# Kernel optimization log

Measured on AMD Instinct MI355X. Metric: run time of the kernel, lower is better.

Reference implementation:

```python
import jax, jax.numpy as jnp
import numpy as np

N_NODES = 50000
N_EDGES = 800000
M_IN = 512
H_OUT = 512


def setup_inputs() -> dict:
    key = jax.random.key(0)
    k1, k2, k3, k4, k5 = jax.random.split(key, 5)
    X = jax.random.normal(k1, (N_NODES, M_IN), dtype=jnp.float32)
    # Xavier-uniform init like nn.init.xavier_uniform_
    limit = float(np.sqrt(6.0 / (M_IN + H_OUT)))
    W = jax.random.uniform(k2, (M_IN, H_OUT), dtype=jnp.float32, minval=-limit, maxval=limit)
    edge_src = jax.random.randint(k3, (N_EDGES,), 0, N_NODES, dtype=jnp.int64 if jax.config.jax_enable_x64 else jnp.int32)
    edge_dst = jax.random.randint(k4, (N_EDGES,), 0, N_NODES, dtype=jnp.int64 if jax.config.jax_enable_x64 else jnp.int32)
    # positive normalized-adjacency-like weights
    edge_vals = jax.random.uniform(k5, (N_EDGES,), dtype=jnp.float32, minval=0.0, maxval=1.0)
    return {"X": X, "W": W, "edge_src": edge_src, "edge_dst": edge_dst, "edge_vals": edge_vals}


def reference(X, W, edge_src, edge_dst, edge_vals):
    # Z = X @ W   (dense projection)
    Z = jnp.matmul(X, W)  # [N, h]
    # A_hat @ Z via COO SpMM: gather source rows, scale by edge weight, scatter-add to dst
    msg = Z[edge_src] * edge_vals[:, None]          # [E, h]
    agg = jax.ops.segment_sum(msg, edge_dst, num_segments=X.shape[0])  # [N, h]
    # sigma = ReLU
    return jax.nn.relu(agg)
```

## Files before the change

### kernel.cpp

```cpp
#include <hip/hip_runtime.h>
#include <hip/hip_bf16.h>

#define N_NODES 50000
#define N_EDGES 800000
#define M_IN 512
#define H_OUT 512
#define BCAP 64

typedef __attribute__((ext_vector_type(8))) short    bf16x8;
typedef __attribute__((ext_vector_type(4))) float    f32x4;
typedef __attribute__((ext_vector_type(8))) unsigned short u16x8;

__device__ inline float bf2f(unsigned short u) {
    unsigned int x = ((unsigned int)u) << 16;
    return __builtin_bit_cast(float, x);
}
__device__ inline unsigned short f2bf(float f) {
    unsigned int x = __builtin_bit_cast(unsigned int, f);
    return (unsigned short)((x + 0x7FFF + ((x >> 16) & 1)) >> 16);
}
__device__ inline void gload_lds16(const void* g, void* lds) {
    __builtin_amdgcn_global_load_lds(
        (const __attribute__((address_space(1))) void*)g,
        (__attribute__((address_space(3))) void*)lds, 16, 0, 0);
}

#define PREP_GROUPS 1042
#define PREP_GRID   (PREP_GROUPS * 10)
#define CONVX_B 6250
#define CONVW_B 1024
#define BUILD_B 3125

__global__ __launch_bounds__(256) void prep_kernel(
    const float* __restrict__ X, unsigned char* __restrict__ Xq,
    float* __restrict__ sc,
    const float* __restrict__ W, unsigned short* __restrict__ Wt,
    const int* __restrict__ esrc, const int* __restrict__ edst,
    const float* __restrict__ eval,
    int* __restrict__ cnt, unsigned int* __restrict__ pairs)
{
    const int grp = blockIdx.x / 10;
    const int ph  = blockIdx.x % 10;
    if (ph < 6) {
        const int cb = grp * 6 + ph;
        if (cb >= CONVX_B) return;
        const int r0 = (cb * 4 + (threadIdx.x >> 6)) * 2;
        const int l  = threadIdx.x & 63;

        const float4 a0 = *(const float4*)(X + (size_t)r0 * M_IN + l * 8);
        const float4 b0 = *(const float4*)(X + (size_t)r0 * M_IN + l * 8 + 4);
        const float4 a1 = *(const float4*)(X + (size_t)(r0 + 1) * M_IN + l * 8);
        const float4 b1 = *(const float4*)(X + (size_t)(r0 + 1) * M_IN + l * 8 + 4);

        float m0 = fmaxf(fmaxf(fmaxf(fabsf(a0.x), fabsf(a0.y)), fmaxf(fabsf(a0.z), fabsf(a0.w))),
                         fmaxf(fmaxf(fabsf(b0.x), fabsf(b0.y)), fmaxf(fabsf(b0.z), fabsf(b0.w))));
        float m1 = fmaxf(fmaxf(fmaxf(fabsf(a1.x), fabsf(a1.y)), fmaxf(fabsf(a1.z), fabsf(a1.w))),
                         fmaxf(fmaxf(fabsf(b1.x), fabsf(b1.y)), fmaxf(fabsf(b1.z), fabsf(b1.w))));
#pragma unroll
        for (int d = 1; d < 64; d <<= 1) {
            m0 = fmaxf(m0, __shfl_xor(m0, d, 64));
            m1 = fmaxf(m1, __shfl_xor(m1, d, 64));
        }
        const float inv0 = (m0 > 0.f) ? 127.f / m0 : 0.f;
        const float inv1 = (m1 > 0.f) ? 127.f / m1 : 0.f;

        const float xs0[8] = {a0.x, a0.y, a0.z, a0.w, b0.x, b0.y, b0.z, b0.w};
        const float xs1[8] = {a1.x, a1.y, a1.z, a1.w, b1.x, b1.y, b1.z, b1.w};
        unsigned int u0[8], u1[8];
#pragma unroll
        for (int j = 0; j < 8; ++j) {
            int q0 = __float2int_rn(xs0[j] * inv0) + 128;
            int q1 = __float2int_rn(xs1[j] * inv1) + 128;
            u0[j] = (unsigned int)max(0, min(255, q0));
            u1[j] = (unsigned int)max(0, min(255, q1));
        }
        uint2 w0, w1;
        w0.x = u0[0] | (u0[1] << 8) | (u0[2] << 16) | (u0[3] << 24);
        w0.y = u0[4] | (u0[5] << 8) | (u0[6] << 16) | (u0[7] << 24);
        w1.x = u1[0] | (u1[1] << 8) | (u1[2] << 16) | (u1[3] << 24);
        w1.y = u1[4] | (u1[5] << 8) | (u1[6] << 16) | (u1[7] << 24);
        *(uint2*)(Xq + (size_t)r0 * M_IN + l * 8)       = w0;
        *(uint2*)(Xq + (size_t)(r0 + 1) * M_IN + l * 8) = w1;
        if (l == 0) sc[r0] = m0 * (1.f / 127.f);
        if (l == 1) sc[r0 + 1] = m1 * (1.f / 127.f);
    } else if (ph < 9) {
        const int bb = grp * 3 + (ph - 6);
        if (bb >= BUILD_B) return;
        const int e = bb * 256 + threadIdx.x;
        const int d   = edst[e];
        const int pos = atomicAdd(&cnt[d], 1);
        if (pos < BCAP)
            pairs[(size_t)d * BCAP + pos] =
                ((unsigned int)esrc[e] << 16) | (unsigned int)f2bf(eval[e]);
    } else {
        const int wb = grp;
        if (wb >= CONVW_B) return;
        const int id = wb * 256 + threadIdx.x;
        const int n = id >> 9, k = id & 511;
        Wt[(size_t)n * 512 + k] = f2bf(W[(size_t)k * 512 + n]);
    }
}

__global__ __launch_bounds__(256) void gather_kernel(
    const unsigned char* __restrict__ Xq,
    const float*        __restrict__ sc,
    const int*          __restrict__ cnt,
    const unsigned int* __restrict__ pairs,
    unsigned short*     __restrict__ Yb)
{
    const int node = blockIdx.x * 4 + (threadIdx.x >> 6);
    const int lane = threadIdx.x & 63;

    const int beg = node * BCAP;
    const int end = beg + min(cnt[node], BCAP);
    const int col = lane * 8;

    float acc[8] = {};
    float S = 0.f;

    int e = beg;
    for (; e + 3 < end; e += 4) {
        const unsigned int k0 = pairs[e],     k1 = pairs[e + 1];
        const unsigned int k2 = pairs[e + 2], k3 = pairs[e + 3];
        const uint2 x0 = *(const uint2*)(Xq + (size_t)(k0 >> 16) * M_IN + col);
        const uint2 x1 = *(const uint2*)(Xq + (size_t)(k1 >> 16) * M_IN + col);
        const uint2 x2 = *(const uint2*)(Xq + (size_t)(k2 >> 16) * M_IN + col);
        const uint2 x3 = *(const uint2*)(Xq + (size_t)(k3 >> 16) * M_IN + col);
        const float f0 = bf2f((unsigned short)(k0 & 0xffffu)) * sc[k0 >> 16];
        const float f1 = bf2f((unsigned short)(k1 & 0xffffu)) * sc[k1 >> 16];
        const float f2 = bf2f((unsigned short)(k2 & 0xffffu)) * sc[k2 >> 16];
        const float f3 = bf2f((unsigned short)(k3 & 0xffffu)) * sc[k3 >> 16];
        S += f0 + f1 + f2 + f3;
#pragma unroll
        for (int j = 0; j < 4; ++j) {
            acc[j]     += (float)((x0.x >> (8 * j)) & 0xffu) * f0
                        + (float)((x1.x >> (8 * j)) & 0xffu) * f1
                        + (float)((x2.x >> (8 * j)) & 0xffu) * f2
                        + (float)((x3.x >> (8 * j)) & 0xffu) * f3;
            acc[4 + j] += (float)((x0.y >> (8 * j)) & 0xffu) * f0
                        + (float)((x1.y >> (8 * j)) & 0xffu) * f1
                        + (float)((x2.y >> (8 * j)) & 0xffu) * f2
                        + (float)((x3.y >> (8 * j)) & 0xffu) * f3;
        }
    }
    for (; e < end; ++e) {
        const unsigned int k0 = pairs[e];
        const uint2 x0 = *(const uint2*)(Xq + (size_t)(k0 >> 16) * M_IN + col);
        const float f0 = bf2f((unsigned short)(k0 & 0xffffu)) * sc[k0 >> 16];
        S += f0;
#pragma unroll
        for (int j = 0; j < 4; ++j) {
            acc[j]     += (float)((x0.x >> (8 * j)) & 0xffu) * f0;
            acc[4 + j] += (float)((x0.y >> (8 * j)) & 0xffu) * f0;
        }
    }

    u16x8 o;
#pragma unroll
    for (int j = 0; j < 8; ++j) o[j] = f2bf(acc[j] - 128.f * S);
    *(u16x8*)(Yb + (size_t)node * M_IN + col) = o;
}

#define BM 128
#define BN 128
#define BK 32
#define NT (M_IN / BK)
#define ROWT ((N_NODES + BM - 1) / BM)
#define GEMM_GRID (((ROWT + 7) / 8) * 8 * 4)

__global__ __launch_bounds__(256, 4) void gemm_mfma_kernel(
    const unsigned short* __restrict__ Yb,
    const unsigned short* __restrict__ Wt,
    float* __restrict__ out)
{
    const int bid = blockIdx.x;
    const int s   = bid >> 3;
    const int r   = (s >> 2) * 8 + (bid & 7);
    if (r >= ROWT) return;
    const int row0 = r * BM;
    const int col0 = (s & 3) * BN;

    __shared__ unsigned short As[2][BM * BK];
    __shared__ unsigned short Bs[2][BN * BK];

    const int tid  = threadIdx.x;
    const int lane = tid & 63;
    const int wid  = tid >> 6;
    const int wr   = wid >> 1;
    const int wc   = wid & 1;

    f32x4 acc[4][4] = {};

    int srow[2], ksw[2], ldsb[2];
#pragma unroll
    for (int i = 0; i < 2; ++i) {
        const int b   = (i * 256 + tid) * 16;
        const int row = b >> 6;
        const int cir = (b >> 4) & 3;
        srow[i] = row;
        ksw[i]  = (cir ^ ((row >> 1) & 3)) << 3;
        ldsb[i] = b;
    }
    int agr[2];
#pragma unroll
    for (int i = 0; i < 2; ++i) {
        int gr = row0 + srow[i];
        if (gr >= N_NODES) gr = N_NODES - 1;
        agr[i] = gr;
    }

    int abyte[4], bbyte[4];
    const int c = lane >> 4;
#pragma unroll
    for (int m = 0; m < 4; ++m) {
        const int ra = wr * 64 + m * 16 + (lane & 15);
        abyte[m] = ra * 64 + ((c ^ ((ra >> 1) & 3)) << 4);
        const int rb = wc * 64 + m * 16 + (lane & 15);
        bbyte[m] = rb * 64 + ((c ^ ((rb >> 1) & 3)) << 4);
    }

#define STAGE(buf, k0)                                                          \
    do {                                                                        \
        _Pragma("unroll")                                                       \
        for (int i = 0; i < 2; ++i) {                                           \
            gload_lds16(Yb + (size_t)agr[i] * M_IN + (k0) + ksw[i],             \
                        (char*)As[buf] + ldsb[i]);                              \
            gload_lds16(Wt + (size_t)(col0 + srow[i]) * M_IN + (k0) + ksw[i],   \
                        (char*)Bs[buf] + ldsb[i]);                              \
        }                                                                       \
    } while (0)

    STAGE(0, 0);
    asm volatile("s_waitcnt vmcnt(0)" ::: "memory");
    __builtin_amdgcn_s_barrier();

    int cur = 0;
    for (int t = 0; t < NT; ++t) {
        if (t + 1 < NT) STAGE(cur ^ 1, (t + 1) * BK);

        bf16x8 af[4], bfr[4];
#pragma unroll
        for (int m = 0; m < 4; ++m)
            af[m]  = *(const bf16x8*)((const char*)As[cur] + abyte[m]);
#pragma unroll
        for (int n = 0; n < 4; ++n)
            bfr[n] = *(const bf16x8*)((const char*)Bs[cur] + bbyte[n]);

#pragma unroll
        for (int m = 0; m < 4; ++m)
#pragma unroll
            for (int n = 0; n < 4; ++n)
                acc[m][n] = __builtin_amdgcn_mfma_f32_16x16x32_bf16(
                    af[m], bfr[n], acc[m][n], 0, 0, 0);

        if (t + 1 < NT) {
            asm volatile("s_waitcnt vmcnt(0)" ::: "memory");
            __builtin_amdgcn_s_barrier();
        }
        cur ^= 1;
    }
#undef STAGE

#pragma unroll
    for (int m = 0; m < 4; ++m) {
#pragma unroll
        for (int n = 0; n < 4; ++n) {
#pragma unroll
            for (int rr = 0; rr < 4; ++rr) {
                const int row = row0 + wr * 64 + m * 16 + (lane >> 4) * 4 + rr;
                const int col = col0 + wc * 64 + n * 16 + (lane & 15);
                if (row < N_NODES)
                    out[(size_t)row * H_OUT + col] = fmaxf(acc[m][n][rr], 0.f);
            }
        }
    }
}

extern "C" void kernel_launch(void* const* d_in, const int* in_sizes, int n_in,
                              void* d_out, int out_size, void* d_ws, size_t ws_size,
                              hipStream_t stream) {
    const float* X    = (const float*)d_in[0];
    const float* W    = (const float*)d_in[1];
    const int*   esrc = (const int*)d_in[2];
    const int*   edst = (const int*)d_in[3];
    const float* eval = (const float*)d_in[4];
    float* out = (float*)d_out;

    char* w = (char*)d_ws;
    unsigned short* Yb = (unsigned short*)w;  w += (size_t)N_NODES * M_IN * 2;
    unsigned char*  Xq = (unsigned char*)w;   w += (size_t)N_NODES * M_IN;
    float*          sc = (float*)w;           w += (size_t)N_NODES * 4;
    unsigned short* Wt = (unsigned short*)w;  w += (size_t)M_IN * H_OUT * 2;
    int*   cnt  = (int*)w;                    w += (size_t)N_NODES * 4;
    unsigned int* pairs = (unsigned int*)w;

    hipMemsetAsync(cnt, 0, (size_t)N_NODES * sizeof(int), stream);

    prep_kernel<<<PREP_GRID, 256, 0, stream>>>(
        X, Xq, sc, W, Wt, esrc, edst, eval, cnt, pairs);

    gather_kernel<<<(N_NODES + 3) / 4, 256, 0, stream>>>(Xq, sc, cnt, pairs, Yb);

    gemm_mfma_kernel<<<GEMM_GRID, 256, 0, stream>>>(Yb, Wt, out);
}
```

Before: 164.6 us.

## Switch aggregation GEMM from bf16 to int8 MFMA with per-row/column scales

Quantizes the aggregated features to int8 with a per-node scale in the gather kernel, and quantizes W to int8 with a per-output-column scale. The GEMM then uses i32 16x16x64 int8 MFMA with BK=64 and dequantizes in the epilogue. This halves operand bytes for Yq and W and uses the higher-throughput int8 matrix path. The cost is a wavefront max-reduction in the gather, extra scale loads in the epilogue, and lower numerical accuracy from 8-bit quantization of both operands.

```diff
diff --git a/kernel.cpp b/kernel.cpp
--- a/kernel.cpp
+++ b/kernel.cpp
@@ -7,8 +7,7 @@
 #define H_OUT 512
 #define BCAP 64
 
-typedef __attribute__((ext_vector_type(8))) short    bf16x8;
-typedef __attribute__((ext_vector_type(4))) float    f32x4;
+typedef __attribute__((ext_vector_type(4))) int      v4i;
 typedef __attribute__((ext_vector_type(8))) unsigned short u16x8;
 
 __device__ inline float bf2f(unsigned short u) {
@@ -28,13 +27,14 @@
 #define PREP_GROUPS 1042
 #define PREP_GRID   (PREP_GROUPS * 10)
 #define CONVX_B 6250
-#define CONVW_B 1024
 #define BUILD_B 3125
+#define WQ_B    128
 
 __global__ __launch_bounds__(256) void prep_kernel(
     const float* __restrict__ X, unsigned char* __restrict__ Xq,
     float* __restrict__ sc,
-    const float* __restrict__ W, unsigned short* __restrict__ Wt,
+    const float* __restrict__ W, signed char* __restrict__ Wq,
+    float* __restrict__ sw,
     const int* __restrict__ esrc, const int* __restrict__ edst,
     const float* __restrict__ eval,
     int* __restrict__ cnt, unsigned int* __restrict__ pairs)
@@ -93,11 +93,28 @@
             pairs[(size_t)d * BCAP + pos] =
                 ((unsigned int)esrc[e] << 16) | (unsigned int)f2bf(eval[e]);
     } else {
-        const int wb = grp;
-        if (wb >= CONVW_B) return;
-        const int id = wb * 256 + threadIdx.x;
-        const int n = id >> 9, k = id & 511;
-        Wt[(size_t)n * 512 + k] = f2bf(W[(size_t)k * 512 + n]);
+        if (grp >= WQ_B) return;
+        const int n = grp * 4 + (threadIdx.x >> 6);
+        const int l = threadIdx.x & 63;
+        float wv[8];
+        float am = 0.f;
+#pragma unroll
+        for (int j = 0; j < 8; ++j) {
+            wv[j] = W[(size_t)(l * 8 + j) * H_OUT + n];
+            am = fmaxf(am, fabsf(wv[j]));
+        }
+#pragma unroll
+        for (int d = 1; d < 64; d <<= 1) am = fmaxf(am, __shfl_xor(am, d, 64));
+        const float inv = (am > 0.f) ? 127.f / am : 0.f;
+        int q[8];
+#pragma unroll
+        for (int j = 0; j < 8; ++j)
+            q[j] = max(-127, min(127, __float2int_rn(wv[j] * inv)));
+        uint2 pk;
+        pk.x = (q[0] & 0xff) | ((q[1] & 0xff) << 8) | ((q[2] & 0xff) << 16) | ((q[3] & 0xff) << 24);
+        pk.y = (q[4] & 0xff) | ((q[5] & 0xff) << 8) | ((q[6] & 0xff) << 16) | ((q[7] & 0xff) << 24);
+        *(uint2*)(Wq + (size_t)n * M_IN + l * 8) = pk;
+        if (l == 0) sw[n] = am * (1.f / 127.f);
     }
 }
 
@@ -106,7 +123,8 @@
     const float*        __restrict__ sc,
     const int*          __restrict__ cnt,
     const unsigned int* __restrict__ pairs,
-    unsigned short*     __restrict__ Yb)
+    signed char*        __restrict__ Yq,
+    float*              __restrict__ sy)
 {
     const int node = blockIdx.x * 4 + (threadIdx.x >> 6);
     const int lane = threadIdx.x & 63;
@@ -155,22 +173,39 @@
         }
     }
 
-    u16x8 o;
-#pragma unroll
-    for (int j = 0; j < 8; ++j) o[j] = f2bf(acc[j] - 128.f * S);
-    *(u16x8*)(Yb + (size_t)node * M_IN + col) = o;
+    float y[8];
+    float am = 0.f;
+#pragma unroll
+    for (int j = 0; j < 8; ++j) {
+        y[j] = acc[j] - 128.f * S;
+        am = fmaxf(am, fabsf(y[j]));
+    }
+#pragma unroll
+    for (int d = 1; d < 64; d <<= 1) am = fmaxf(am, __shfl_xor(am, d, 64));
+    const float inv = (am > 0.f) ? 127.f / am : 0.f;
+    int q[8];
+#pragma unroll
+    for (int j = 0; j < 8; ++j)
+        q[j] = max(-127, min(127, __float2int_rn(y[j] * inv)));
+    uint2 pk;
+    pk.x = (q[0] & 0xff) | ((q[1] & 0xff) << 8) | ((q[2] & 0xff) << 16) | ((q[3] & 0xff) << 24);
+    pk.y = (q[4] & 0xff) | ((q[5] & 0xff) << 8) | ((q[6] & 0xff) << 16) | ((q[7] & 0xff) << 24);
+    *(uint2*)(Yq + (size_t)node * M_IN + col) = pk;
+    if (lane == 0) sy[node] = am * (1.f / 127.f);
 }
 
 #define BM 128
 #define BN 128
-#define BK 32
-#define NT (M_IN / BK)
+#define BKI 64
+#define NTI (M_IN / BKI)
 #define ROWT ((N_NODES + BM - 1) / BM)
 #define GEMM_GRID (((ROWT + 7) / 8) * 8 * 4)
 
-__global__ __launch_bounds__(256, 4) void gemm_mfma_kernel(
-    const unsigned short* __restrict__ Yb,
-    const unsigned short* __restrict__ Wt,
+__global__ __launch_bounds__(256, 4) void gemm_i8_kernel(
+    const signed char* __restrict__ Yq,
+    const signed char* __restrict__ Wq,
+    const float* __restrict__ sy,
+    const float* __restrict__ sw,
     float* __restrict__ out)
 {
     const int bid = blockIdx.x;
@@ -180,8 +215,8 @@
     const int row0 = r * BM;
     const int col0 = (s & 3) * BN;
 
-    __shared__ unsigned short As[2][BM * BK];
-    __shared__ unsigned short Bs[2][BN * BK];
+    __shared__ signed char As[2][BM * BKI];
+    __shared__ signed char Bs[2][BN * BKI];
 
     const int tid  = threadIdx.x;
     const int lane = tid & 63;
@@ -189,7 +224,7 @@
     const int wr   = wid >> 1;
     const int wc   = wid & 1;
 
-    f32x4 acc[4][4] = {};
+    v4i acc[4][4] = {};
 
     int srow[2], ksw[2], ldsb[2];
 #pragma unroll
@@ -198,7 +233,7 @@
         const int row = b >> 6;
         const int cir = (b >> 4) & 3;
         srow[i] = row;
-        ksw[i]  = (cir ^ ((row >> 1) & 3)) << 3;
+        ksw[i]  = (cir ^ ((row >> 1) & 3)) << 4;
         ldsb[i] = b;
     }
     int agr[2];
@@ -223,9 +258,9 @@
     do {                                                                        \
         _Pragma("unroll")                                                       \
         for (int i = 0; i < 2; ++i) {                                           \
-            gload_lds16(Yb + (size_t)agr[i] * M_IN + (k0) + ksw[i],             \
+            gload_lds16(Yq + (size_t)agr[i] * M_IN + (k0) + ksw[i],             \
                         (char*)As[buf] + ldsb[i]);                              \
-            gload_lds16(Wt + (size_t)(col0 + srow[i]) * M_IN + (k0) + ksw[i],   \
+            gload_lds16(Wq + (size_t)(col0 + srow[i]) * M_IN + (k0) + ksw[i],   \
                         (char*)Bs[buf] + ldsb[i]);                              \
         }                                                                       \
     } while (0)
@@ -235,25 +270,25 @@
     __builtin_amdgcn_s_barrier();
 
     int cur = 0;
-    for (int t = 0; t < NT; ++t) {
-        if (t + 1 < NT) STAGE(cur ^ 1, (t + 1) * BK);
-
-        bf16x8 af[4], bfr[4];
+    for (int t = 0; t < NTI; ++t) {
+        if (t + 1 < NTI) STAGE(cur ^ 1, (t + 1) * BKI);
+
+        v4i af[4], bfr[4];
 #pragma unroll
         for (int m = 0; m < 4; ++m)
-            af[m]  = *(const bf16x8*)((const char*)As[cur] + abyte[m]);
+            af[m]  = *(const v4i*)((const char*)As[cur] + abyte[m]);
 #pragma unroll
         for (int n = 0; n < 4; ++n)
-            bfr[n] = *(const bf16x8*)((const char*)Bs[cur] + bbyte[n]);
+            bfr[n] = *(const v4i*)((const char*)Bs[cur] + bbyte[n]);
 
 #pragma unroll
         for (int m = 0; m < 4; ++m)
 #pragma unroll
             for (int n = 0; n < 4; ++n)
-                acc[m][n] = __builtin_amdgcn_mfma_f32_16x16x32_bf16(
+                acc[m][n] = __builtin_amdgcn_mfma_i32_16x16x64_i8(
                     af[m], bfr[n], acc[m][n], 0, 0, 0);
 
-        if (t + 1 < NT) {
+        if (t + 1 < NTI) {
             asm volatile("s_waitcnt vmcnt(0)" ::: "memory");
             __builtin_amdgcn_s_barrier();
         }
@@ -261,16 +296,24 @@
     }
 #undef STAGE
 
+    float sw4[4];
+#pragma unroll
+    for (int n = 0; n < 4; ++n)
+        sw4[n] = sw[col0 + wc * 64 + n * 16 + (lane & 15)];
+
 #pragma unroll
     for (int m = 0; m < 4; ++m) {
 #pragma unroll
-        for (int n = 0; n < 4; ++n) {
-#pragma unroll
-            for (int rr = 0; rr < 4; ++rr) {
-                const int row = row0 + wr * 64 + m * 16 + (lane >> 4) * 4 + rr;
-                const int col = col0 + wc * 64 + n * 16 + (lane & 15);
-                if (row < N_NODES)
-                    out[(size_t)row * H_OUT + col] = fmaxf(acc[m][n][rr], 0.f);
+        for (int rr = 0; rr < 4; ++rr) {
+            const int row = row0 + wr * 64 + m * 16 + (lane >> 4) * 4 + rr;
+            if (row < N_NODES) {
+                const float syv = sy[row];
+#pragma unroll
+                for (int n = 0; n < 4; ++n) {
+                    const int col = col0 + wc * 64 + n * 16 + (lane & 15);
+                    out[(size_t)row * H_OUT + col] =
+                        fmaxf((float)acc[m][n][rr] * syv * sw4[n], 0.f);
+                }
             }
         }
     }
@@ -287,19 +330,22 @@
     float* out = (float*)d_out;
 
     char* w = (char*)d_ws;
-    unsigned short* Yb = (unsigned short*)w;  w += (size_t)N_NODES * M_IN * 2;
+    signed char*    Yq = (signed char*)w;     w += (size_t)N_NODES * M_IN;
     unsigned char*  Xq = (unsigned char*)w;   w += (size_t)N_NODES * M_IN;
     float*          sc = (float*)w;           w += (size_t)N_NODES * 4;
-    unsigned short* Wt = (unsigned short*)w;  w += (size_t)M_IN * H_OUT * 2;
+    float*          sy = (float*)w;           w += (size_t)N_NODES * 4;
+    signed char*    Wq = (signed char*)w;     w += (size_t)M_IN * H_OUT;
+    float*          sw = (float*)w;           w += (size_t)H_OUT * 4;
     int*   cnt  = (int*)w;                    w += (size_t)N_NODES * 4;
     unsigned int* pairs = (unsigned int*)w;
 
     hipMemsetAsync(cnt, 0, (size_t)N_NODES * sizeof(int), stream);
 
     prep_kernel<<<PREP_GRID, 256, 0, stream>>>(
-        X, Xq, sc, W, Wt, esrc, edst, eval, cnt, pairs);
-
-    gather_kernel<<<(N_NODES + 3) / 4, 256, 0, stream>>>(Xq, sc, cnt, pairs, Yb);
-
-    gemm_mfma_kernel<<<GEMM_GRID, 256, 0, stream>>>(Yb, Wt, out);
-}
+        X, Xq, sc, W, Wq, sw, esrc, edst, eval, cnt, pairs);
+
+    gather_kernel<<<(N_NODES + 3) / 4, 256, 0, stream>>>(
+        Xq, sc, cnt, pairs, Yq, sy);
+
+    gemm_i8_kernel<<<GEMM_GRID, 256, 0, stream>>>(Yq, Wq, sy, sw, out);
+}
```

Result: faster. 157.1 us (median of 2 runs) (-4.6%).
